# Optimization experiments

Hardware: AMD Instinct MI355X
Metric: run time of the kernel (lower is better)

## Reference

```python
import jax, jax.numpy as jnp
import numpy as np

N_GOAL, N_OBS, N_TASK = 16384, 65536, 8192
E1, E2 = 1048576, 1048576
B = 256            # graphs in batch
F, S = 128, 64     # dim_features, dim_state


def setup_inputs() -> dict:
    key = jax.random.key(0)
    ks = jax.random.split(key, 16)
    inp = {
        "x_goal": jax.random.normal(ks[0], (N_GOAL, F), jnp.float32),
        "x_obs": jax.random.normal(ks[1], (N_OBS, F), jnp.float32),
        "x_task": jax.random.normal(ks[2], (N_TASK, S), jnp.float32),
        "ei_go_src": jax.random.randint(ks[3], (E1,), 0, N_GOAL),
        "ei_go_dst": jax.random.randint(ks[4], (E1,), 0, N_OBS),
        "ei_ot_src": jax.random.randint(ks[5], (E2,), 0, N_OBS),
        "ei_ot_dst": jax.random.randint(ks[6], (E2,), 0, N_TASK),
        # contiguous graph assignment: 32 task nodes per graph
        "task_batch": jnp.arange(N_TASK) // (N_TASK // B),
        # GinStandardMLP (state_gin): Lin(F,S)-ReLU-Lin(S,S)-ReLU
        "W1": jax.random.normal(ks[7], (F, S), jnp.float32) * 0.05,
        "b1": jnp.zeros((S,), jnp.float32),
        "W2": jax.random.normal(ks[8], (S, S), jnp.float32) * 0.05,
        "b2": jnp.zeros((S,), jnp.float32),
        # GinUnactivatedMLP (action_gin): Lin(S,S)-ReLU-Lin(S,1)
        "W3": jax.random.normal(ks[9], (S, S), jnp.float32) * 0.05,
        "b3": jnp.zeros((S,), jnp.float32),
        "W4": jax.random.normal(ks[10], (S, 1), jnp.float32) * 0.05,
        "b4": jnp.zeros((1,), jnp.float32),
        # critic head: Lin(2,8)-ReLU-Lin(8,1)
        "Wc1": jax.random.normal(ks[11], (2, 8), jnp.float32) * 0.5,
        "bc1": jnp.zeros((8,), jnp.float32),
        "Wc2": jax.random.normal(ks[12], (8, 1), jnp.float32) * 0.5,
        "bc2": jnp.zeros((1,), jnp.float32),
    }
    return inp


def reference(x_goal, x_obs, x_task,
              ei_go_src, ei_go_dst, ei_ot_src, ei_ot_dst, task_batch,
              W1, b1, W2, b2, W3, b3, W4, b4, Wc1, bc1, Wc2, bc2):
    # --- state_gin: GINConv((goal, obs)), eps=0 ---
    agg1 = jax.ops.segment_sum(x_goal[ei_go_src], ei_go_dst, num_segments=N_OBS)
    h = x_obs + agg1                              # (1+eps)*x_dst + sum_j x_src
    h = jax.nn.relu(h @ W1 + b1)
    x1 = jax.nn.relu(h @ W2 + b2)                 # [N_OBS, S]

    # --- action_gin: GINConv((obs, task)), eps=0 ---
    agg2 = jax.ops.segment_sum(x1[ei_ot_src], ei_ot_dst, num_segments=N_TASK)
    g = x_task + agg2
    g = jax.nn.relu(g @ W3 + b3)
    x2 = g @ W4 + b4                              # [N_TASK, 1]

    # --- critic path: global max / mean pool over task nodes per graph ---
    max_pool = jax.ops.segment_max(x2, task_batch, num_segments=B)   # [B, 1]
    cnt = jax.ops.segment_sum(jnp.ones((N_TASK, 1), x2.dtype), task_batch, num_segments=B)
    mean_pool = jax.ops.segment_sum(x2, task_batch, num_segments=B) / cnt  # [B, 1]

    pooled = jnp.concatenate([max_pool.max(axis=1, keepdims=True),
                              mean_pool.mean(axis=1, keepdims=True)], axis=1)  # [B, 2]
    out = jax.nn.relu(pooled @ Wc1 + bc1) @ Wc2 + bc2                 # [B, 1]
    return out.squeeze(-1)                                            # [B]
```

## Files before the change

kernel.cpp:

```cpp
#include <hip/hip_runtime.h>
#include <hip/hip_bf16.h>


#define CAP1 2816
#define CAP2 5120
#define GEMM_BLKS 640

__global__ __launch_bounds__(256) void prep(
    const float* __restrict__ x_goal, const float* __restrict__ x_obs,
    const float* __restrict__ W, float* __restrict__ xg1,
    float* __restrict__ obs,
    const int* __restrict__ go_src, const int* __restrict__ go_dst,
    const int* __restrict__ ot_src, const int* __restrict__ ot_dst,
    int* __restrict__ gcur1, int* __restrict__ gcur2,
    int* __restrict__ pairs1, int* __restrict__ pairs2, int nblk1)
{
    __shared__ float smem[8192];
    const int tid = threadIdx.x;

    if (blockIdx.x < GEMM_BLKS) {
        const float* X;
        float* O;
        int row0;
        if (blockIdx.x < 128) { X = x_goal; O = xg1; row0 = blockIdx.x * 128; }
        else                  { X = x_obs;  O = obs; row0 = (blockIdx.x - 128) * 128; }
        const int c0 = (tid & 7) * 8;
        const int trow = tid >> 3;
        const int r0 = trow * 4;
        const int swz = trow & 7;
        const int w = tid >> 6;
        const int lane = tid & 63;
        const int srow = w * 32 + (lane >> 3);
        const int skbx = lane & 7;

        float acc[4][8];
        #pragma unroll
        for (int i = 0; i < 4; ++i)
            #pragma unroll
            for (int j = 0; j < 8; ++j) acc[i][j] = 0.f;

        float* bufA = smem;
        float* bufB = smem + 4096;

        auto stage = [&](float* buf, int k0) {
            #pragma unroll
            for (int m = 0; m < 4; ++m) {
                int row = srow + m * 8;
                int kg = skbx ^ ((row >> 2) & 7);
                const float* gp = X + (size_t)(row0 + row) * 128 + k0 + kg * 4;
                __builtin_amdgcn_global_load_lds(
                    (const __attribute__((address_space(1))) unsigned int*)gp,
                    (__attribute__((address_space(3))) unsigned int*)
                        (buf + (w * 4 + m) * 256),
                    16, 0, 0);
            }
        };

        stage(bufA, 0);
        __syncthreads();

        float* cur = bufA;
        float* nxt = bufB;
        for (int kc = 0; kc < 4; ++kc) {
            const int k0 = kc * 32;
            if (kc < 3) stage(nxt, k0 + 32);
            #pragma unroll 2
            for (int kb = 0; kb < 8; ++kb) {
                float4 xv[4];
                #pragma unroll
                for (int i = 0; i < 4; ++i)
                    xv[i] = *(const float4*)(cur + (r0 + i) * 32 + ((kb ^ swz) << 2));
                #pragma unroll
                for (int kk = 0; kk < 4; ++kk) {
                    const float* wp = W + (size_t)(k0 + kb * 4 + kk) * 64 + c0;
                    float4 w0 = *(const float4*)(wp);
                    float4 w1 = *(const float4*)(wp + 4);
                    #pragma unroll
                    for (int i = 0; i < 4; ++i) {
                        float xk = (kk == 0) ? xv[i].x : (kk == 1) ? xv[i].y
                                 : (kk == 2) ? xv[i].z : xv[i].w;
                        acc[i][0] = fmaf(xk, w0.x, acc[i][0]);
                        acc[i][1] = fmaf(xk, w0.y, acc[i][1]);
                        acc[i][2] = fmaf(xk, w0.z, acc[i][2]);
                        acc[i][3] = fmaf(xk, w0.w, acc[i][3]);
                        acc[i][4] = fmaf(xk, w1.x, acc[i][4]);
                        acc[i][5] = fmaf(xk, w1.y, acc[i][5]);
                        acc[i][6] = fmaf(xk, w1.z, acc[i][6]);
                        acc[i][7] = fmaf(xk, w1.w, acc[i][7]);
                    }
                }
            }
            __syncthreads();
            float* t = cur; cur = nxt; nxt = t;
        }
        #pragma unroll
        for (int i = 0; i < 4; ++i) {
            float4 o0; o0.x = acc[i][0]; o0.y = acc[i][1]; o0.z = acc[i][2]; o0.w = acc[i][3];
            float4 o1; o1.x = acc[i][4]; o1.y = acc[i][5]; o1.z = acc[i][6]; o1.w = acc[i][7];
            float* p = O + (size_t)(row0 + r0 + i) * 64 + c0;
            *(float4*)p = o0;
            *(float4*)(p + 4) = o1;
        }
    } else {
        int* hist = (int*)smem;
        int* cur  = (int*)smem + 512;
        const int blk2 = blockIdx.x - GEMM_BLKS;
        const bool s1 = blk2 < nblk1;
        const int* src = s1 ? go_src : ot_src;
        const int* dst = s1 ? go_dst : ot_dst;
        int* gcur  = s1 ? gcur1 : gcur2;
        int* pairs = s1 ? pairs1 : pairs2;
        const int bsh  = s1 ? 7 : 5;
        const int rowm = s1 ? 127 : 31;
        const int nb   = s1 ? 512 : 256;
        const int cap  = s1 ? CAP1 : CAP2;
        const int blk  = s1 ? blk2 : blk2 - nblk1;

        for (int i = tid; i < nb; i += 256) hist[i] = 0;
        __syncthreads();
        const int base = blk * 4096;
        const int4* d4 = (const int4*)(dst + base);
        const int4* s4 = (const int4*)(src + base);
        int4 dv[4];
        #pragma unroll
        for (int k = 0; k < 4; ++k) {
            dv[k] = d4[k * 256 + tid];
            atomicAdd(&hist[dv[k].x >> bsh], 1);
            atomicAdd(&hist[dv[k].y >> bsh], 1);
            atomicAdd(&hist[dv[k].z >> bsh], 1);
            atomicAdd(&hist[dv[k].w >> bsh], 1);
        }
        __syncthreads();
        for (int i = tid; i < nb; i += 256)
            cur[i] = atomicAdd(&gcur[i], hist[i]);
        __syncthreads();
        #pragma unroll
        for (int k = 0; k < 4; ++k) {
            int4 sv = s4[k * 256 + tid];
            int d, s, b, p;
            d = dv[k].x; s = sv.x; b = d >> bsh; p = atomicAdd(&cur[b], 1);
            if (p < cap) pairs[(size_t)b * cap + p] = ((d & rowm) << 17) | s;
            d = dv[k].y; s = sv.y; b = d >> bsh; p = atomicAdd(&cur[b], 1);
            if (p < cap) pairs[(size_t)b * cap + p] = ((d & rowm) << 17) | s;
            d = dv[k].z; s = sv.z; b = d >> bsh; p = atomicAdd(&cur[b], 1);
            if (p < cap) pairs[(size_t)b * cap + p] = ((d & rowm) << 17) | s;
            d = dv[k].w; s = sv.w; b = d >> bsh; p = atomicAdd(&cur[b], 1);
            if (p < cap) pairs[(size_t)b * cap + p] = ((d & rowm) << 17) | s;
        }
    }
}

__global__ __launch_bounds__(1024) void gather_mlp_obs(
    const int* __restrict__ pairs, const int* __restrict__ cnt,
    const float* __restrict__ xg1, const float* __restrict__ obs,
    const float* __restrict__ b1, const float* __restrict__ W2,
    const float* __restrict__ b2, float* __restrict__ x1)
{
    constexpr int ROWS = 128;
    __shared__ int ssrc[CAP1];
    __shared__ int offs[ROWS + 1];
    __shared__ int rcnt[ROWS];
    __shared__ float W2t[64 * 68];
    __shared__ float hb[16 * 64];
    const int tid = threadIdx.x;
    const int b = blockIdx.x;

    #pragma unroll
    for (int i = tid; i < 4096; i += 1024) {
        int k = i >> 6, c = i & 63;
        W2t[c * 68 + k] = W2[i];
    }
    if (tid < ROWS) rcnt[tid] = 0;
    __syncthreads();
    int n = cnt[b];
    if (n > CAP1) n = CAP1;
    const int* bp = pairs + (size_t)b * CAP1;

    int e0 = -1, e1 = -1, e2 = -1;
    {
        int i = tid;
        if (i < n) {
            e0 = bp[i]; atomicAdd(&rcnt[e0 >> 17], 1); i += 1024;
            if (i < n) {
                e1 = bp[i]; atomicAdd(&rcnt[e1 >> 17], 1); i += 1024;
                if (i < n) { e2 = bp[i]; atomicAdd(&rcnt[e2 >> 17], 1); }
            }
        }
    }
    __syncthreads();
    if (tid < 64) {
        int v0 = rcnt[2 * tid], v1 = rcnt[2 * tid + 1];
        int s = v0 + v1;
        #pragma unroll
        for (int d = 1; d < 64; d <<= 1) {
            int t = __shfl_up(s, d);
            if (tid >= d) s += t;
        }
        int ex = s - v0 - v1;
        offs[2 * tid] = ex;
        offs[2 * tid + 1] = ex + v0;
        rcnt[2 * tid] = ex;
        rcnt[2 * tid + 1] = ex + v0;
        if (tid == 63) offs[ROWS] = s;
    }
    __syncthreads();
    if (e0 >= 0) { int p = atomicAdd(&rcnt[e0 >> 17], 1); ssrc[p] = e0 & 0x1FFFF; }
    if (e1 >= 0) { int p = atomicAdd(&rcnt[e1 >> 17], 1); ssrc[p] = e1 & 0x1FFFF; }
    if (e2 >= 0) { int p = atomicAdd(&rcnt[e2 >> 17], 1); ssrc[p] = e2 & 0x1FFFF; }
    __syncthreads();
    const int wv = tid >> 6;
    const int lane = tid & 63;
    const float bb1 = b1[lane];
    const float bb2 = b2[lane];
    float* hp = hb + wv * 64;
    const float4* h4 = (const float4*)hp;
    const float4* wrow = (const float4*)(W2t + lane * 68);
    for (int r = wv; r < ROWS; r += 16) {
        int beg = offs[r], end = offs[r + 1];
        float a0 = 0.f, a1 = 0.f, a2 = 0.f, a3 = 0.f;
        int e = beg;
        for (; e + 4 <= end; e += 4) {
            int s0 = ssrc[e], s1 = ssrc[e + 1], s2 = ssrc[e + 2], s3 = ssrc[e + 3];
            a0 += xg1[(size_t)s0 * 64 + lane];
            a1 += xg1[(size_t)s1 * 64 + lane];
            a2 += xg1[(size_t)s2 * 64 + lane];
            a3 += xg1[(size_t)s3 * 64 + lane];
        }
        for (; e < end; ++e)
            a0 += xg1[(size_t)ssrc[e] * 64 + lane];
        size_t gi = (((size_t)b * ROWS) + r) * 64 + lane;
        float acc = (a0 + a1) + (a2 + a3) + obs[gi];
        hp[lane] = fmaxf(acc + bb1, 0.f);
        float a = bb2;
        #pragma unroll 8
        for (int kc = 0; kc < 16; ++kc) {
            float4 hv = h4[kc];
            float4 wv4 = wrow[kc];
            a = fmaf(hv.x, wv4.x, a);
            a = fmaf(hv.y, wv4.y, a);
            a = fmaf(hv.z, wv4.z, a);
            a = fmaf(hv.w, wv4.w, a);
        }
        x1[gi] = fmaxf(a, 0.f);
    }
}

__global__ __launch_bounds__(1024) void gather_mlp_task_pool(
    const int* __restrict__ pairs, const int* __restrict__ cnt,
    const float* __restrict__ x1, const float* __restrict__ x_task,
    const float* __restrict__ W3, const float* __restrict__ b3,
    const float* __restrict__ W4, const float* __restrict__ b4,
    const float* __restrict__ Wc1, const float* __restrict__ bc1,
    const float* __restrict__ Wc2, const float* __restrict__ bc2,
    float* __restrict__ out)
{
    constexpr int ROWS = 32;
    __shared__ int ssrc[CAP2];
    __shared__ int offs[ROWS + 1];
    __shared__ int rcnt[ROWS];
    __shared__ float W3t[64 * 68];
    __shared__ float hb[16 * 64];
    __shared__ float xrow[ROWS];
    const int tid = threadIdx.x;
    const int b = blockIdx.x;

    #pragma unroll
    for (int i = tid; i < 4096; i += 1024) {
        int k = i >> 6, c = i & 63;
        W3t[c * 68 + k] = W3[i];
    }
    if (tid < ROWS) rcnt[tid] = 0;
    __syncthreads();
    int n = cnt[b];
    if (n > CAP2) n = CAP2;
    const int* bp = pairs + (size_t)b * CAP2;

    int e0 = -1, e1 = -1, e2 = -1, e3 = -1, e4 = -1;
    {
        int i = tid;
        if (i < n) { e0 = bp[i]; atomicAdd(&rcnt[e0 >> 17], 1); i += 1024;
        if (i < n) { e1 = bp[i]; atomicAdd(&rcnt[e1 >> 17], 1); i += 1024;
        if (i < n) { e2 = bp[i]; atomicAdd(&rcnt[e2 >> 17], 1); i += 1024;
        if (i < n) { e3 = bp[i]; atomicAdd(&rcnt[e3 >> 17], 1); i += 1024;
        if (i < n) { e4 = bp[i]; atomicAdd(&rcnt[e4 >> 17], 1); } } } } }
    }
    __syncthreads();
    if (tid < 32) {
        int v = rcnt[tid];
        int s = v;
        #pragma unroll
        for (int d = 1; d < 32; d <<= 1) {
            int t = __shfl_up(s, d);
            if (tid >= d) s += t;
        }
        int ex = s - v;
        offs[tid] = ex;
        rcnt[tid] = ex;
        if (tid == 31) offs[ROWS] = s;
    }
    __syncthreads();
    if (e0 >= 0) { int p = atomicAdd(&rcnt[e0 >> 17], 1); ssrc[p] = e0 & 0x1FFFF; }
    if (e1 >= 0) { int p = atomicAdd(&rcnt[e1 >> 17], 1); ssrc[p] = e1 & 0x1FFFF; }
    if (e2 >= 0) { int p = atomicAdd(&rcnt[e2 >> 17], 1); ssrc[p] = e2 & 0x1FFFF; }
    if (e3 >= 0) { int p = atomicAdd(&rcnt[e3 >> 17], 1); ssrc[p] = e3 & 0x1FFFF; }
    if (e4 >= 0) { int p = atomicAdd(&rcnt[e4 >> 17], 1); ssrc[p] = e4 & 0x1FFFF; }
    __syncthreads();

    const int wv = tid >> 6;
    const int lane = tid & 63;
    const float bb3 = b3[lane];
    const float w4l = W4[lane];
    const float b4c = b4[0];
    float* hp = hb + wv * 64;
    const float4* h4 = (const float4*)hp;
    const float4* wrow = (const float4*)(W3t + lane * 68);
    #pragma unroll
    for (int half = 0; half < 2; ++half) {
        const int r = wv + half * 16;
        const int row = b * ROWS + r;
        int beg = offs[r], end = offs[r + 1];
        float a0 = 0.f, a1 = 0.f, a2 = 0.f, a3 = 0.f;
        float a4 = 0.f, a5 = 0.f, a6 = 0.f, a7 = 0.f;
        int e = beg;
        for (; e + 8 <= end; e += 8) {
            int s0 = ssrc[e],     s1 = ssrc[e + 1], s2 = ssrc[e + 2], s3 = ssrc[e + 3];
            int s4 = ssrc[e + 4], s5 = ssrc[e + 5], s6 = ssrc[e + 6], s7 = ssrc[e + 7];
            a0 += x1[(size_t)s0 * 64 + lane];
            a1 += x1[(size_t)s1 * 64 + lane];
            a2 += x1[(size_t)s2 * 64 + lane];
            a3 += x1[(size_t)s3 * 64 + lane];
            a4 += x1[(size_t)s4 * 64 + lane];
            a5 += x1[(size_t)s5 * 64 + lane];
            a6 += x1[(size_t)s6 * 64 + lane];
            a7 += x1[(size_t)s7 * 64 + lane];
        }
        for (; e < end; ++e)
            a0 += x1[(size_t)ssrc[e] * 64 + lane];
        float t = ((a0 + a1) + (a2 + a3)) + ((a4 + a5) + (a6 + a7))
                + x_task[(size_t)row * 64 + lane];
        hp[lane] = t;
        float a = bb3;
        #pragma unroll 8
        for (int kc = 0; kc < 16; ++kc) {
            float4 hv = h4[kc];
            float4 wv4 = wrow[kc];
            a = fmaf(hv.x, wv4.x, a);
            a = fmaf(hv.y, wv4.y, a);
            a = fmaf(hv.z, wv4.z, a);
            a = fmaf(hv.w, wv4.w, a);
        }
        float p = fmaxf(a, 0.f) * w4l;
        p += __shfl_xor(p, 1);
        p += __shfl_xor(p, 2);
        p += __shfl_xor(p, 4);
        p += __shfl_xor(p, 8);
        p += __shfl_xor(p, 16);
        p += __shfl_xor(p, 32);
        if (lane == 0) xrow[r] = p + b4c;
    }
    __syncthreads();
    if (tid == 0) {
        float mx = -1e30f, sm = 0.f;
        #pragma unroll
        for (int i = 0; i < ROWS; ++i) {
            float v = xrow[i];
            mx = fmaxf(mx, v);
            sm += v;
        }
        float mn = sm * (1.f / 32.f);
        float o = bc2[0];
        #pragma unroll
        for (int j = 0; j < 8; ++j) {
            float t = fmaxf(mx * Wc1[j] + mn * Wc1[8 + j] + bc1[j], 0.f);
            o = fmaf(t, Wc2[j], o);
        }
        out[b] = o;
    }
}

extern "C" void kernel_launch(void* const* d_in, const int* in_sizes, int n_in,
                              void* d_out, int out_size, void* d_ws, size_t ws_size,
                              hipStream_t stream)
{
    const float* x_goal = (const float*)d_in[0];
    const float* x_obs  = (const float*)d_in[1];
    const float* x_task = (const float*)d_in[2];
    const int* go_src = (const int*)d_in[3];
    const int* go_dst = (const int*)d_in[4];
    const int* ot_src = (const int*)d_in[5];
    const int* ot_dst = (const int*)d_in[6];
    const float* W1  = (const float*)d_in[8];
    const float* b1  = (const float*)d_in[9];
    const float* W2  = (const float*)d_in[10];
    const float* b2  = (const float*)d_in[11];
    const float* W3  = (const float*)d_in[12];
    const float* b3  = (const float*)d_in[13];
    const float* W4  = (const float*)d_in[14];
    const float* b4  = (const float*)d_in[15];
    const float* Wc1 = (const float*)d_in[16];
    const float* bc1 = (const float*)d_in[17];
    const float* Wc2 = (const float*)d_in[18];
    const float* bc2 = (const float*)d_in[19];
    float* out = (float*)d_out;

    const int N_OBS = 65536, N_GOAL = 16384;
    const int E1 = in_sizes[3], E2 = in_sizes[5];
    const int NB1 = 512, NB2 = 256;

    char* w = (char*)d_ws;
    float* obs    = (float*)w;  w += (size_t)N_OBS * 64 * 4;
    float* x1     = (float*)w;  w += (size_t)N_OBS * 64 * 4;
    float* xg1    = (float*)w;  w += (size_t)N_GOAL * 64 * 4;
    int*   pairs1 = (int*)w;    w += (size_t)NB1 * CAP1 * 4;
    int*   pairs2 = (int*)w;    w += (size_t)NB2 * CAP2 * 4;
    int*   gcur1  = (int*)w;    w += NB1 * 4;
    int*   gcur2  = (int*)w;    w += NB2 * 4;

    hipMemsetAsync(gcur1, 0, (NB1 + NB2) * 4, stream);

    const int nblk1 = E1 / 4096;
    const int nblk2 = E2 / 4096;
    prep<<<GEMM_BLKS + nblk1 + nblk2, 256, 0, stream>>>(
        x_goal, x_obs, W1, xg1, obs,
        go_src, go_dst, ot_src, ot_dst, gcur1, gcur2, pairs1, pairs2, nblk1);
    gather_mlp_obs<<<NB1, 1024, 0, stream>>>(pairs1, gcur1, xg1, obs, b1, W2, b2, x1);
    gather_mlp_task_pool<<<NB2, 1024, 0, stream>>>(pairs2, gcur2, x1, x_task,
                                                   W3, b3, W4, b4,
                                                   Wc1, bc1, Wc2, bc2, out);
}
```

Baseline: 232.6 us.

## Batch per-warp matvec over multiple rows, pre-transpose weights once, vectorize index loads

The W2/W3 transpose now runs once in an extra prep block and writes a padded layout to a workspace, so each gather block does a plain coalesced copy instead of a strided transpose into shared memory. Each wavefront gathers four rows (obs) or two rows (task) before running the second-layer matvec, so each W row loaded from shared memory is reused across several rows. Source indices are read as int4 from shared memory after an alignment prologue. The cost is a larger per-warp staging buffer in shared memory and more registers held across the gather phase.

Result: slower. 252.9 us (+8.7%).

```diff
diff --git a/kernel.cpp b/kernel.cpp
--- a/kernel.cpp
+++ b/kernel.cpp
@@ -13,7 +13,9 @@
     const int* __restrict__ go_src, const int* __restrict__ go_dst,
     const int* __restrict__ ot_src, const int* __restrict__ ot_dst,
     int* __restrict__ gcur1, int* __restrict__ gcur2,
-    int* __restrict__ pairs1, int* __restrict__ pairs2, int nblk1)
+    int* __restrict__ pairs1, int* __restrict__ pairs2, int nblk1, int nblk2,
+    const float* __restrict__ W2, const float* __restrict__ W3,
+    float* __restrict__ w2t_g, float* __restrict__ w3t_g)
 {
     __shared__ float smem[8192];
     const int tid = threadIdx.x;
@@ -101,7 +103,7 @@
             *(float4*)p = o0;
             *(float4*)(p + 4) = o1;
         }
-    } else {
+    } else if (blockIdx.x < GEMM_BLKS + nblk1 + nblk2) {
         int* hist = (int*)smem;
         int* cur  = (int*)smem + 512;
         const int blk2 = blockIdx.x - GEMM_BLKS;
@@ -147,29 +149,34 @@
             d = dv[k].w; s = sv.w; b = d >> bsh; p = atomicAdd(&cur[b], 1);
             if (p < cap) pairs[(size_t)b * cap + p] = ((d & rowm) << 17) | s;
         }
+    } else {
+        for (int i = tid; i < 4352; i += 256) {
+            int c = i / 68, k = i % 68;
+            float v2 = (k < 64) ? W2[k * 64 + c] : 0.f;
+            float v3 = (k < 64) ? W3[k * 64 + c] : 0.f;
+            w2t_g[i] = v2;
+            w3t_g[i] = v3;
+        }
     }
 }
 
 __global__ __launch_bounds__(1024) void gather_mlp_obs(
     const int* __restrict__ pairs, const int* __restrict__ cnt,
     const float* __restrict__ xg1, const float* __restrict__ obs,
-    const float* __restrict__ b1, const float* __restrict__ W2,
+    const float* __restrict__ b1, const float* __restrict__ w2t_g,
     const float* __restrict__ b2, float* __restrict__ x1)
 {
     constexpr int ROWS = 128;
-    __shared__ int ssrc[CAP1];
+    __shared__ __align__(16) int ssrc[CAP1];
     __shared__ int offs[ROWS + 1];
     __shared__ int rcnt[ROWS];
-    __shared__ float W2t[64 * 68];
-    __shared__ float hb[16 * 64];
+    __shared__ __align__(16) float W2t[64 * 68];
+    __shared__ __align__(16) float hb[16 * 4 * 64];
     const int tid = threadIdx.x;
     const int b = blockIdx.x;
 
     #pragma unroll
-    for (int i = tid; i < 4096; i += 1024) {
-        int k = i >> 6, c = i & 63;
-        W2t[c * 68 + k] = W2[i];
-    }
+    for (int i = tid; i < 4352; i += 1024) W2t[i] = w2t_g[i];
     if (tid < ROWS) rcnt[tid] = 0;
     __syncthreads();
     int n = cnt[b];
@@ -212,63 +219,75 @@
     const int lane = tid & 63;
     const float bb1 = b1[lane];
     const float bb2 = b2[lane];
-    float* hp = hb + wv * 64;
-    const float4* h4 = (const float4*)hp;
+    float* hpg = hb + wv * 256;
+    const float4* h40 = (const float4*)hpg;
     const float4* wrow = (const float4*)(W2t + lane * 68);
-    for (int r = wv; r < ROWS; r += 16) {
-        int beg = offs[r], end = offs[r + 1];
-        float a0 = 0.f, a1 = 0.f, a2 = 0.f, a3 = 0.f;
-        int e = beg;
-        for (; e + 4 <= end; e += 4) {
-            int s0 = ssrc[e], s1 = ssrc[e + 1], s2 = ssrc[e + 2], s3 = ssrc[e + 3];
-            a0 += xg1[(size_t)s0 * 64 + lane];
-            a1 += xg1[(size_t)s1 * 64 + lane];
-            a2 += xg1[(size_t)s2 * 64 + lane];
-            a3 += xg1[(size_t)s3 * 64 + lane];
-        }
-        for (; e < end; ++e)
-            a0 += xg1[(size_t)ssrc[e] * 64 + lane];
-        size_t gi = (((size_t)b * ROWS) + r) * 64 + lane;
-        float acc = (a0 + a1) + (a2 + a3) + obs[gi];
-        hp[lane] = fmaxf(acc + bb1, 0.f);
-        float a = bb2;
-        #pragma unroll 8
+    #pragma unroll
+    for (int g = 0; g < 2; ++g) {
+        const int rbase = wv + g * 64;
+        #pragma unroll
+        for (int j = 0; j < 4; ++j) {
+            int r = rbase + j * 16;
+            int beg = offs[r], end = offs[r + 1];
+            float a0 = 0.f, a1 = 0.f, a2 = 0.f, a3 = 0.f;
+            int e = beg;
+            for (; e < end && (e & 3); ++e)
+                a0 += xg1[(size_t)ssrc[e] * 64 + lane];
+            for (; e + 4 <= end; e += 4) {
+                int4 ss = *(const int4*)(ssrc + e);
+                a0 += xg1[(size_t)ss.x * 64 + lane];
+                a1 += xg1[(size_t)ss.y * 64 + lane];
+                a2 += xg1[(size_t)ss.z * 64 + lane];
+                a3 += xg1[(size_t)ss.w * 64 + lane];
+            }
+            for (; e < end; ++e)
+                a0 += xg1[(size_t)ssrc[e] * 64 + lane];
+            size_t gi = (((size_t)b * ROWS) + r) * 64 + lane;
+            float acc = (a0 + a1) + (a2 + a3) + obs[gi];
+            hpg[j * 64 + lane] = fmaxf(acc + bb1, 0.f);
+        }
+        float acc4[4] = {bb2, bb2, bb2, bb2};
+        #pragma unroll 4
         for (int kc = 0; kc < 16; ++kc) {
-            float4 hv = h4[kc];
             float4 wv4 = wrow[kc];
-            a = fmaf(hv.x, wv4.x, a);
-            a = fmaf(hv.y, wv4.y, a);
-            a = fmaf(hv.z, wv4.z, a);
-            a = fmaf(hv.w, wv4.w, a);
-        }
-        x1[gi] = fmaxf(a, 0.f);
+            #pragma unroll
+            for (int j = 0; j < 4; ++j) {
+                float4 hv = h40[j * 16 + kc];
+                acc4[j] = fmaf(hv.x, wv4.x, acc4[j]);
+                acc4[j] = fmaf(hv.y, wv4.y, acc4[j]);
+                acc4[j] = fmaf(hv.z, wv4.z, acc4[j]);
+                acc4[j] = fmaf(hv.w, wv4.w, acc4[j]);
+            }
+        }
+        #pragma unroll
+        for (int j = 0; j < 4; ++j) {
+            size_t gi = (((size_t)b * ROWS) + rbase + j * 16) * 64 + lane;
+            x1[gi] = fmaxf(acc4[j], 0.f);
+        }
     }
 }
 
 __global__ __launch_bounds__(1024) void gather_mlp_task_pool(
     const int* __restrict__ pairs, const int* __restrict__ cnt,
     const float* __restrict__ x1, const float* __restrict__ x_task,
-    const float* __restrict__ W3, const float* __restrict__ b3,
+    const float* __restrict__ w3t_g, const float* __restrict__ b3,
     const float* __restrict__ W4, const float* __restrict__ b4,
     const float* __restrict__ Wc1, const float* __restrict__ bc1,
     const float* __restrict__ Wc2, const float* __restrict__ bc2,
     float* __restrict__ out)
 {
     constexpr int ROWS = 32;
-    __shared__ int ssrc[CAP2];
+    __shared__ __align__(16) int ssrc[CAP2];
     __shared__ int offs[ROWS + 1];
     __shared__ int rcnt[ROWS];
-    __shared__ float W3t[64 * 68];
-    __shared__ float hb[16 * 64];
+    __shared__ __align__(16) float W3t[64 * 68];
+    __shared__ __align__(16) float hb[16 * 2 * 64];
     __shared__ float xrow[ROWS];
     const int tid = threadIdx.x;
     const int b = blockIdx.x;
 
     #pragma unroll
-    for (int i = tid; i < 4096; i += 1024) {
-        int k = i >> 6, c = i & 63;
-        W3t[c * 68 + k] = W3[i];
-    }
+    for (int i = tid; i < 4352; i += 1024) W3t[i] = w3t_g[i];
     if (tid < ROWS) rcnt[tid] = 0;
     __syncthreads();
     int n = cnt[b];
@@ -311,8 +330,8 @@
     const float bb3 = b3[lane];
     const float w4l = W4[lane];
     const float b4c = b4[0];
-    float* hp = hb + wv * 64;
-    const float4* h4 = (const float4*)hp;
+    float* hpg = hb + wv * 128;
+    const float4* h40 = (const float4*)hpg;
     const float4* wrow = (const float4*)(W3t + lane * 68);
     #pragma unroll
     for (int half = 0; half < 2; ++half) {
@@ -322,41 +341,60 @@
         float a0 = 0.f, a1 = 0.f, a2 = 0.f, a3 = 0.f;
         float a4 = 0.f, a5 = 0.f, a6 = 0.f, a7 = 0.f;
         int e = beg;
+        for (; e < end && (e & 3); ++e)
+            a0 += x1[(size_t)ssrc[e] * 64 + lane];
         for (; e + 8 <= end; e += 8) {
-            int s0 = ssrc[e],     s1 = ssrc[e + 1], s2 = ssrc[e + 2], s3 = ssrc[e + 3];
-            int s4 = ssrc[e + 4], s5 = ssrc[e + 5], s6 = ssrc[e + 6], s7 = ssrc[e + 7];
-            a0 += x1[(size_t)s0 * 64 + lane];
-            a1 += x1[(size_t)s1 * 64 + lane];
-            a2 += x1[(size_t)s2 * 64 + lane];
-            a3 += x1[(size_t)s3 * 64 + lane];
-            a4 += x1[(size_t)s4 * 64 + lane];
-            a5 += x1[(size_t)s5 * 64 + lane];
-            a6 += x1[(size_t)s6 * 64 + lane];
-            a7 += x1[(size_t)s7 * 64 + lane];
+            int4 s0 = *(const int4*)(ssrc + e);
+            int4 s1 = *(const int4*)(ssrc + e + 4);
+            a0 += x1[(size_t)s0.x * 64 + lane];
+            a1 += x1[(size_t)s0.y * 64 + lane];
+            a2 += x1[(size_t)s0.z * 64 + lane];
+            a3 += x1[(size_t)s0.w * 64 + lane];
+            a4 += x1[(size_t)s1.x * 64 + lane];
+            a5 += x1[(size_t)s1.y * 64 + lane];
+            a6 += x1[(size_t)s1.z * 64 + lane];
+            a7 += x1[(size_t)s1.w * 64 + lane];
+        }
+        for (; e + 4 <= end; e += 4) {
+            int4 s0 = *(const int4*)(ssrc + e);
+            a0 += x1[(size_t)s0.x * 64 + lane];
+            a1 += x1[(size_t)s0.y * 64 + lane];
+            a2 += x1[(size_t)s0.z * 64 + lane];
+            a3 += x1[(size_t)s0.w * 64 + lane];
         }
         for (; e < end; ++e)
             a0 += x1[(size_t)ssrc[e] * 64 + lane];
         float t = ((a0 + a1) + (a2 + a3)) + ((a4 + a5) + (a6 + a7))
                 + x_task[(size_t)row * 64 + lane];
-        hp[lane] = t;
-        float a = bb3;
-        #pragma unroll 8
+        hpg[half * 64 + lane] = t;
+    }
+    {
+        float acc2[2] = {bb3, bb3};
+        #pragma unroll 4
         for (int kc = 0; kc < 16; ++kc) {
-            float4 hv = h4[kc];
             float4 wv4 = wrow[kc];
-            a = fmaf(hv.x, wv4.x, a);
-            a = fmaf(hv.y, wv4.y, a);
-            a = fmaf(hv.z, wv4.z, a);
-            a = fmaf(hv.w, wv4.w, a);
-        }
-        float p = fmaxf(a, 0.f) * w4l;
-        p += __shfl_xor(p, 1);
-        p += __shfl_xor(p, 2);
-        p += __shfl_xor(p, 4);
-        p += __shfl_xor(p, 8);
-        p += __shfl_xor(p, 16);
-        p += __shfl_xor(p, 32);
-        if (lane == 0) xrow[r] = p + b4c;
+            float4 hv0 = h40[kc];
+            float4 hv1 = h40[16 + kc];
+            acc2[0] = fmaf(hv0.x, wv4.x, acc2[0]);
+            acc2[0] = fmaf(hv0.y, wv4.y, acc2[0]);
+            acc2[0] = fmaf(hv0.z, wv4.z, acc2[0]);
+            acc2[0] = fmaf(hv0.w, wv4.w, acc2[0]);
+            acc2[1] = fmaf(hv1.x, wv4.x, acc2[1]);
+            acc2[1] = fmaf(hv1.y, wv4.y, acc2[1]);
+            acc2[1] = fmaf(hv1.z, wv4.z, acc2[1]);
+            acc2[1] = fmaf(hv1.w, wv4.w, acc2[1]);
+        }
+        #pragma unroll
+        for (int half = 0; half < 2; ++half) {
+            float p = fmaxf(acc2[half], 0.f) * w4l;
+            p += __shfl_xor(p, 1);
+            p += __shfl_xor(p, 2);
+            p += __shfl_xor(p, 4);
+            p += __shfl_xor(p, 8);
+            p += __shfl_xor(p, 16);
+            p += __shfl_xor(p, 32);
+            if (lane == 0) xrow[wv + half * 16] = p + b4c;
+        }
     }
     __syncthreads();
     if (tid == 0) {
@@ -415,16 +453,19 @@
     int*   pairs2 = (int*)w;    w += (size_t)NB2 * CAP2 * 4;
     int*   gcur1  = (int*)w;    w += NB1 * 4;
     int*   gcur2  = (int*)w;    w += NB2 * 4;
+    float* w2t_g  = (float*)w;  w += 64 * 68 * 4;
+    float* w3t_g  = (float*)w;  w += 64 * 68 * 4;
 
     hipMemsetAsync(gcur1, 0, (NB1 + NB2) * 4, stream);
 
     const int nblk1 = E1 / 4096;
     const int nblk2 = E2 / 4096;
-    prep<<<GEMM_BLKS + nblk1 + nblk2, 256, 0, stream>>>(
+    prep<<<GEMM_BLKS + nblk1 + nblk2 + 1, 256, 0, stream>>>(
         x_goal, x_obs, W1, xg1, obs,
-        go_src, go_dst, ot_src, ot_dst, gcur1, gcur2, pairs1, pairs2, nblk1);
-    gather_mlp_obs<<<NB1, 1024, 0, stream>>>(pairs1, gcur1, xg1, obs, b1, W2, b2, x1);
+        go_src, go_dst, ot_src, ot_dst, gcur1, gcur2, pairs1, pairs2,
+        nblk1, nblk2, W2, W3, w2t_g, w3t_g);
+    gather_mlp_obs<<<NB1, 1024, 0, stream>>>(pairs1, gcur1, xg1, obs, b1, w2t_g, b2, x1);
     gather_mlp_task_pool<<<NB2, 1024, 0, stream>>>(pairs2, gcur2, x1, x_task,
-                                                   W3, b3, W4, b4,
+                                                   w3t_g, b3, W4, b4,
                                                    Wc1, bc1, Wc2, bc2, out);
 }
```
